# Optimization experiments

Hardware: AMD Instinct MI355X
Metric: run time of the kernel (lower is better)

The kernel has to match this reference:

```python
import jax, jax.numpy as jnp
import numpy as np

B, H, W = 128, 64, 64
MAP = 128          # gff mapping_dim
GFF_SCALE = 10.0   # common default scale for Gaussian Fourier features


def _ku(k, shape, fan_in):
    # torch kaiming_uniform_(a=sqrt(5)) -> bound = 1/sqrt(fan_in)
    b = 1.0 / np.sqrt(fan_in)
    return jax.random.uniform(k, shape, jnp.float32, -b, b)


def setup_inputs() -> dict:
    key = jax.random.key(0)
    ks = jax.random.split(key, 16)
    coords = jax.random.uniform(ks[0], (B, 2, H, W), jnp.float32)
    Bmat = GFF_SCALE * jax.random.normal(ks[1], (2, MAP), jnp.float32)
    # FMMLinear(256, 256_out? no) -- linear1: in=256, out=256, rank=70
    L1 = _ku(ks[2], (256, 70), 70)
    R1 = _ku(ks[3], (70, 256), 256)
    b1 = jax.random.uniform(ks[4], (256,), jnp.float32, -1/np.sqrt(256), 1/np.sqrt(256))
    # linear2: in=256, out=128, rank=10
    L2 = _ku(ks[5], (128, 10), 10)
    R2 = _ku(ks[6], (10, 256), 256)
    b2 = jax.random.uniform(ks[7], (128,), jnp.float32, -1/np.sqrt(256), 1/np.sqrt(256))
    # dense layers (torch nn.Linear default init)
    W3 = _ku(ks[8], (32, 128), 128)
    b3 = jax.random.uniform(ks[9], (32,), jnp.float32, -1/np.sqrt(128), 1/np.sqrt(128))
    W4 = _ku(ks[10], (16, 32), 32)
    b4 = jax.random.uniform(ks[11], (16,), jnp.float32, -1/np.sqrt(32), 1/np.sqrt(32))
    W5 = _ku(ks[12], (3, 16), 16)
    b5 = jax.random.uniform(ks[13], (3,), jnp.float32, -1/np.sqrt(16), 1/np.sqrt(16))
    return dict(coords=coords, Bmat=Bmat, L1=L1, R1=R1, b1=b1,
                L2=L2, R2=R2, b2=b2, W3=W3, b3=b3, W4=W4, b4=b4, W5=W5, b5=b5)


def reference(coords, Bmat, L1, R1, b1, L2, R2, b2, W3, b3, W4, b4, W5, b5):
    # Gaussian Fourier features: [B,2,H,W] -> [B,H,W,2*MAP]
    proj = (2.0 * jnp.pi) * jnp.einsum('bchw,cm->bhwm', coords, Bmat)
    x = jnp.concatenate([jnp.sin(proj), jnp.cos(proj)], axis=-1)
    x = x.reshape(-1, 2 * MAP)                       # (b h w) c
    x = jax.nn.relu(x @ (L1 @ R1).T + b1)            # FMM linear1
    x = jax.nn.relu(x @ (L2 @ R2).T + b2)            # FMM linear2
    x = jax.nn.relu(x @ W3.T + b3)
    x = jax.nn.relu(x @ W4.T + b4)
    out = (x @ W5.T + b5)[None]                      # [1, B*H*W, 3]
    return out
```

## Files before the change

kernel.cpp:

```cpp
#include <hip/hip_runtime.h>


typedef __attribute__((ext_vector_type(8))) short bf16x8;
typedef __attribute__((ext_vector_type(4))) float f32x4;
typedef __attribute__((ext_vector_type(4))) int i32x4;

__device__ inline unsigned short f2bf(float f) {
  unsigned u = __float_as_uint(f);
  return (unsigned short)((u + 0x7FFFu + ((u >> 16) & 1u)) >> 16);
}
__device__ inline unsigned short f2bf_fast(float f) {
  return (unsigned short)((__float_as_uint(f) + 0x8000u) >> 16);
}
__device__ inline unsigned packbf(float s, float c) {
  return (unsigned)((__float_as_uint(s) + 0x8000u) >> 16) |
         ((__float_as_uint(c) + 0x8000u) & 0xFFFF0000u);
}

__global__ __launch_bounds__(256) void prep_pack(
    const float* __restrict__ R1, const float* __restrict__ L1,
    const float* __restrict__ R2, const float* __restrict__ L2,
    const float* __restrict__ W3, const float* __restrict__ W4,
    void* __restrict__ ws) {
  unsigned short* w16 = (unsigned short*)ws;
  float* wf = (float*)ws;
  int e = blockIdx.x * 256 + threadIdx.x;
  if (e < 20480) {
    int kt = e / 2560, rem = e % 2560;
    int n = rem >> 5, oj = rem & 31;
    int k = kt * 32 + oj;
    int feat = (k & 1) ? 128 + (k >> 1) : (k >> 1);
    w16[e] = f2bf((n < 70) ? R1[n * 256 + feat] : 0.0f);
  } else if (e < 45056) {
    int f = e - 20480;
    int kt = f / 8192, rem = f % 8192;
    int n = rem >> 5, oj = rem & 31;
    int k = kt * 32 + oj;
    w16[e] = f2bf((k < 70) ? L1[n * 70 + k] : 0.0f);
  } else if (e < 49152) {
    int f = e - 45056;
    int kt = f / 512, rem = f % 512;
    int n = rem >> 5, k = kt * 32 + (rem & 31);
    w16[e] = f2bf((n < 10) ? R2[n * 256 + k] : 0.0f);
  } else if (e < 53248) {
    int f = e - 49152;
    int j = f & 7, h = (f >> 3) & 3, n = (f >> 5) & 15, nt = f >> 9;
    int k = h * 8 + j;
    w16[e] = f2bf((k < 10) ? L2[(nt * 16 + n) * 10 + k] : 0.0f);
  } else if (e < 57344) {
    int f = e - 53248;
    int j = f & 7, h = (f >> 3) & 3, n = (f >> 5) & 15;
    int nt2 = (f >> 9) & 1, rd = f >> 10;
    w16[e] = f2bf(W3[(nt2 * 16 + n) * 128 + rd * 32 + h * 8 + j]);
  } else if (e < 57856) {
    int h2 = e - 57344;
    int q = h2 >> 4, p = h2 & 15;
    wf[28672 + h2] = W4[p * 32 + q];
  }
}

__global__ __launch_bounds__(64, 2) void mlp_mfma(
    const float* __restrict__ coords, const float* __restrict__ Bm,
    const float* __restrict__ b1, const float* __restrict__ b2,
    const float* __restrict__ b3v, const float* __restrict__ b4v,
    const float* __restrict__ W5, const float* __restrict__ b5,
    const void* __restrict__ ws, float* __restrict__ out) {
  const int l = threadIdx.x;
  const int lo = l & 15, hi = l >> 4;
  const int pix0 = blockIdx.x * 64;

  __shared__ __align__(16) char smem[13312];
  unsigned short* Y16 = (unsigned short*)smem;
  unsigned short* X16 = (unsigned short*)smem;
  unsigned short* Z16 = (unsigned short*)(smem + 5632);
  float* O3f = (float*)smem;

  const unsigned short* R1p = (const unsigned short*)ws;
  const unsigned short* L1p = ((const unsigned short*)ws) + 20480;
  const unsigned short* R2p = ((const unsigned short*)ws) + 45056;
  const unsigned short* L2p = ((const unsigned short*)ws) + 49152;
  const unsigned short* W3p = ((const unsigned short*)ws) + 53248;
  const float* W4T = ((const float*)ws) + 28672;

  const f32x4 fz = {0.0f, 0.0f, 0.0f, 0.0f};

  float c0m[4], c1m[4];
#pragma unroll
  for (int mt = 0; mt < 4; ++mt) {
    int p = pix0 + mt * 16 + lo;
    int bb = p >> 12, hw = p & 4095;
    c0m[mt] = coords[bb * 8192 + hw];
    c1m[mt] = coords[bb * 8192 + 4096 + hw];
  }

  f32x4 y[4][5];
#pragma unroll
  for (int mt = 0; mt < 4; ++mt)
#pragma unroll
    for (int nt = 0; nt < 5; ++nt) y[mt][nt] = fz;

  float bm0[4], bm1[4];
#pragma unroll
  for (int p = 0; p < 4; ++p) {
    int m = hi * 4 + p;
    bm0[p] = Bm[m]; bm1[p] = Bm[128 + m];
  }
  for (int kt = 0; kt < 8; ++kt) {
    float nb0[4], nb1[4];
    if (kt < 7) {
#pragma unroll
      for (int p = 0; p < 4; ++p) {
        int m = (kt + 1) * 16 + hi * 4 + p;
        nb0[p] = Bm[m]; nb1[p] = Bm[128 + m];
      }
    }
    bf16x8 bfr[5];
#pragma unroll
    for (int nt = 0; nt < 5; ++nt)
      bfr[nt] = *(const bf16x8*)(R1p + ((kt * 80 + nt * 16 + lo) * 4 + hi) * 8);
    bf16x8 af[4];
#pragma unroll
    for (int mt = 0; mt < 4; ++mt) {
#pragma unroll
      for (int p = 0; p < 4; ++p) {
        float u = fmaf(c0m[mt], bm0[p], c1m[mt] * bm1[p]);
        float t = u - floorf(u);
        float s = __builtin_amdgcn_sinf(t);
        float c = __builtin_amdgcn_cosf(t);
        ((unsigned*)&af[mt])[p] = packbf(s, c);
      }
    }
#pragma unroll
    for (int mt = 0; mt < 4; ++mt)
#pragma unroll
      for (int nt = 0; nt < 5; ++nt)
        y[mt][nt] = __builtin_amdgcn_mfma_f32_16x16x32_bf16(af[mt], bfr[nt],
                                                            y[mt][nt], 0, 0, 0);
#pragma unroll
    for (int p = 0; p < 4; ++p) { bm0[p] = nb0[p]; bm1[p] = nb1[p]; }
  }

#pragma unroll
  for (int mt = 0; mt < 4; ++mt)
#pragma unroll
    for (int nt = 0; nt < 5; ++nt)
#pragma unroll
      for (int r = 0; r < 4; ++r)
        Y16[(mt * 16 + hi * 4 + r) * 104 + nt * 16 + lo] = f2bf_fast(y[mt][nt][r]);
  *(i32x4*)(Y16 + l * 104 + 80) = (i32x4){0, 0, 0, 0};
  *(i32x4*)(Y16 + l * 104 + 88) = (i32x4){0, 0, 0, 0};
  __syncthreads();

  bf16x8 ay[4][3];
#pragma unroll
  for (int mt = 0; mt < 4; ++mt)
#pragma unroll
    for (int kt = 0; kt < 3; ++kt)
      ay[mt][kt] = *(const bf16x8*)(Y16 + (mt * 16 + lo) * 104 + kt * 32 + hi * 8);
  __syncthreads();

  f32x4 zfr[4];
#pragma unroll
  for (int mt = 0; mt < 4; ++mt) zfr[mt] = fz;

  bf16x8 blc[3];
#pragma unroll
  for (int kt = 0; kt < 3; ++kt)
    blc[kt] = *(const bf16x8*)(L1p + ((kt * 256 + lo) * 4 + hi) * 8);

#pragma unroll 2
  for (int nt = 0; nt < 16; ++nt) {
    bf16x8 bln[3];
    if (nt < 15) {
#pragma unroll
      for (int kt = 0; kt < 3; ++kt)
        bln[kt] = *(const bf16x8*)(L1p + ((kt * 256 + (nt + 1) * 16 + lo) * 4 + hi) * 8);
    }
    float bias = b1[nt * 16 + lo];
    f32x4 cf[4];
#pragma unroll
    for (int mt = 0; mt < 4; ++mt) cf[mt] = fz;
#pragma unroll
    for (int kt = 0; kt < 3; ++kt)
#pragma unroll
      for (int mt = 0; mt < 4; ++mt)
        cf[mt] = __builtin_amdgcn_mfma_f32_16x16x32_bf16(ay[mt][kt], blc[kt],
                                                         cf[mt], 0, 0, 0);
#pragma unroll
    for (int mt = 0; mt < 4; ++mt)
#pragma unroll
      for (int r = 0; r < 4; ++r)
        X16[(mt * 16 + hi * 4 + r) * 40 + (nt & 1) * 16 + lo] =
            f2bf_fast(fmaxf(cf[mt][r] + bias, 0.0f));
    if (nt & 1) {
      __syncthreads();
      int rd = nt >> 1;
      bf16x8 br = *(const bf16x8*)(R2p + ((rd * 16 + lo) * 4 + hi) * 8);
#pragma unroll
      for (int mt = 0; mt < 4; ++mt) {
        bf16x8 aa = *(const bf16x8*)(X16 + (mt * 16 + lo) * 40 + hi * 8);
        zfr[mt] = __builtin_amdgcn_mfma_f32_16x16x32_bf16(aa, br, zfr[mt],
                                                          0, 0, 0);
      }
      __syncthreads();
    }
#pragma unroll
    for (int kt = 0; kt < 3; ++kt) blc[kt] = bln[kt];
  }

#pragma unroll
  for (int mt = 0; mt < 4; ++mt)
#pragma unroll
    for (int r = 0; r < 4; ++r)
      Z16[(mt * 16 + hi * 4 + r) * 32 + lo] = f2bf_fast(zfr[mt][r]);
  *(i32x4*)(Z16 + l * 32 + 16) = (i32x4){0, 0, 0, 0};
  *(i32x4*)(Z16 + l * 32 + 24) = (i32x4){0, 0, 0, 0};
  __syncthreads();
  bf16x8 az[4];
#pragma unroll
  for (int mt = 0; mt < 4; ++mt)
    az[mt] = *(const bf16x8*)(Z16 + (mt * 16 + lo) * 32 + hi * 8);
  __syncthreads();

  f32x4 o3fr[4][2];
#pragma unroll
  for (int mt = 0; mt < 4; ++mt) { o3fr[mt][0] = fz; o3fr[mt][1] = fz; }

  bf16x8 wlc = *(const bf16x8*)(L2p + (lo * 4 + hi) * 8);
#pragma unroll 2
  for (int nt = 0; nt < 8; ++nt) {
    bf16x8 wln;
    if (nt < 7)
      wln = *(const bf16x8*)(L2p + (((nt + 1) * 16 + lo) * 4 + hi) * 8);
    float bias = b2[nt * 16 + lo];
    f32x4 cf[4];
#pragma unroll
    for (int mt = 0; mt < 4; ++mt)
      cf[mt] = __builtin_amdgcn_mfma_f32_16x16x32_bf16(az[mt], wlc, fz, 0, 0, 0);
#pragma unroll
    for (int mt = 0; mt < 4; ++mt)
#pragma unroll
      for (int r = 0; r < 4; ++r)
        X16[(mt * 16 + hi * 4 + r) * 40 + (nt & 1) * 16 + lo] =
            f2bf_fast(fmaxf(cf[mt][r] + bias, 0.0f));
    if (nt & 1) {
      __syncthreads();
      int rd = nt >> 1;
      bf16x8 aa[4];
#pragma unroll
      for (int mt = 0; mt < 4; ++mt)
        aa[mt] = *(const bf16x8*)(X16 + (mt * 16 + lo) * 40 + hi * 8);
#pragma unroll
      for (int nt2 = 0; nt2 < 2; ++nt2) {
        bf16x8 bw = *(const bf16x8*)(W3p + (((rd * 2 + nt2) * 16 + lo) * 4 + hi) * 8);
#pragma unroll
        for (int mt = 0; mt < 4; ++mt)
          o3fr[mt][nt2] = __builtin_amdgcn_mfma_f32_16x16x32_bf16(
              aa[mt], bw, o3fr[mt][nt2], 0, 0, 0);
      }
      __syncthreads();
    }
    wlc = wln;
  }

#pragma unroll
  for (int mt = 0; mt < 4; ++mt)
#pragma unroll
    for (int nt2 = 0; nt2 < 2; ++nt2)
#pragma unroll
      for (int r = 0; r < 4; ++r)
        O3f[(mt * 16 + hi * 4 + r) * 33 + nt2 * 16 + lo] =
            fmaxf(o3fr[mt][nt2][r] + b3v[nt2 * 16 + lo], 0.0f);
  __syncthreads();

  float o3l[32];
#pragma unroll
  for (int q = 0; q < 32; ++q) o3l[q] = O3f[l * 33 + q];

  float o4[16];
#pragma unroll
  for (int p = 0; p < 16; ++p) o4[p] = b4v[p];
#pragma unroll
  for (int q = 0; q < 32; ++q) {
    float a = o3l[q];
    const float* __restrict__ w4 = W4T + q * 16;
#pragma unroll
    for (int p = 0; p < 16; ++p) o4[p] = fmaf(a, w4[p], o4[p]);
  }
#pragma unroll
  for (int p = 0; p < 16; ++p) o4[p] = fmaxf(o4[p], 0.0f);

#pragma unroll
  for (int e = 0; e < 3; ++e) {
    float acc = b5[e];
    const float* __restrict__ w5 = W5 + e * 16;
#pragma unroll
    for (int p = 0; p < 16; ++p) acc = fmaf(o4[p], w5[p], acc);
    out[(pix0 + l) * 3 + e] = acc;
  }
}

extern "C" void kernel_launch(void* const* d_in, const int* in_sizes, int n_in,
                              void* d_out, int out_size, void* d_ws, size_t ws_size,
                              hipStream_t stream) {
  const float* coords = (const float*)d_in[0];
  const float* Bmat   = (const float*)d_in[1];
  const float* L1     = (const float*)d_in[2];
  const float* R1     = (const float*)d_in[3];
  const float* b1     = (const float*)d_in[4];
  const float* L2     = (const float*)d_in[5];
  const float* R2     = (const float*)d_in[6];
  const float* b2     = (const float*)d_in[7];
  const float* W3     = (const float*)d_in[8];
  const float* b3     = (const float*)d_in[9];
  const float* W4     = (const float*)d_in[10];
  const float* b4     = (const float*)d_in[11];
  const float* W5     = (const float*)d_in[12];
  const float* b5     = (const float*)d_in[13];

  prep_pack<<<227, 256, 0, stream>>>(R1, L1, R2, L2, W3, W4, d_ws);
  mlp_mfma<<<8192, 64, 0, stream>>>(coords, Bmat, b1, b2, b3, b4, W5, b5,
                                    d_ws, (float*)d_out);
}
```

Before: 168.2 us.

## Replace block barriers with per-wave LDS fences and pack bf16 pairs with hardware cvt

Each block now holds two independent waves, and each wave gets its own LDS slice. Because the slices are private, __syncthreads is replaced by s_waitcnt lgkmcnt(0) fences. The weight packing is permuted so that adjacent column pairs interleave, which lets results be written as packed bf16 pairs using the hardware cvt_pk_bf16_f32 when it is available. The intermediate Y tile shrinks by being staged in two passes, and the layer-1 and layer-2 loops now process even and odd column tiles together, double-buffering the X tile. The goals are fewer barriers, fewer LDS stores and higher occupancy. The costs are reliance on wave-local fence semantics, more register pressure, and rounding that may differ slightly from the old software conversion.

Result: slower. 296.5 us (+76.3%).

```diff
diff --git a/kernel.cpp b/kernel.cpp
--- a/kernel.cpp
+++ b/kernel.cpp
@@ -5,17 +5,25 @@
 typedef __attribute__((ext_vector_type(4))) float f32x4;
 typedef __attribute__((ext_vector_type(4))) int i32x4;
 
+#define LFENCE() asm volatile("s_waitcnt lgkmcnt(0)" ::: "memory")
+
 __device__ inline unsigned short f2bf(float f) {
   unsigned u = __float_as_uint(f);
   return (unsigned short)((u + 0x7FFFu + ((u >> 16) & 1u)) >> 16);
 }
-__device__ inline unsigned short f2bf_fast(float f) {
-  return (unsigned short)((__float_as_uint(f) + 0x8000u) >> 16);
-}
-__device__ inline unsigned packbf(float s, float c) {
-  return (unsigned)((__float_as_uint(s) + 0x8000u) >> 16) |
-         ((__float_as_uint(c) + 0x8000u) & 0xFFFF0000u);
-}
+
+#if __has_builtin(__builtin_amdgcn_cvt_pk_bf16_f32)
+typedef __attribute__((ext_vector_type(2))) __bf16 bf16x2;
+__device__ inline unsigned pk2bf(float a, float b) {
+  bf16x2 v = __builtin_amdgcn_cvt_pk_bf16_f32(a, b);
+  return __builtin_bit_cast(unsigned, v);
+}
+#else
+__device__ inline unsigned pk2bf(float a, float b) {
+  return ((__float_as_uint(a) + 0x8000u) >> 16) |
+         ((__float_as_uint(b) + 0x8000u) & 0xFFFF0000u);
+}
+#endif
 
 __global__ __launch_bounds__(256) void prep_pack(
     const float* __restrict__ R1, const float* __restrict__ L1,
@@ -35,13 +43,14 @@
     int f = e - 20480;
     int kt = f / 8192, rem = f % 8192;
     int n = rem >> 5, oj = rem & 31;
-    int k = kt * 32 + oj;
-    w16[e] = f2bf((k < 70) ? L1[n * 70 + k] : 0.0f);
+    int r = kt * 32 + (oj & 1) * 16 + (oj >> 1);
+    w16[e] = f2bf((r < 70) ? L1[n * 70 + r] : 0.0f);
   } else if (e < 49152) {
-    int f = e - 45056;
-    int kt = f / 512, rem = f % 512;
-    int n = rem >> 5, k = kt * 32 + (rem & 31);
-    w16[e] = f2bf((n < 10) ? R2[n * 256 + k] : 0.0f);
+    int g = e - 45056;
+    int rd = g / 512, rem = g % 512;
+    int n = rem >> 5, oj = rem & 31;
+    int j = rd * 32 + (oj & 1) * 16 + (oj >> 1);
+    w16[e] = f2bf((n < 10) ? R2[n * 256 + j] : 0.0f);
   } else if (e < 53248) {
     int f = e - 49152;
     int j = f & 7, h = (f >> 3) & 3, n = (f >> 5) & 15, nt = f >> 9;
@@ -49,9 +58,9 @@
     w16[e] = f2bf((k < 10) ? L2[(nt * 16 + n) * 10 + k] : 0.0f);
   } else if (e < 57344) {
     int f = e - 53248;
-    int j = f & 7, h = (f >> 3) & 3, n = (f >> 5) & 15;
-    int nt2 = (f >> 9) & 1, rd = f >> 10;
-    w16[e] = f2bf(W3[(nt2 * 16 + n) * 128 + rd * 32 + h * 8 + j]);
+    int oj = f & 31, n = (f >> 5) & 15, nt2 = (f >> 9) & 1, rd = f >> 10;
+    int i = rd * 32 + (oj & 1) * 16 + (oj >> 1);
+    w16[e] = f2bf(W3[(nt2 * 16 + n) * 128 + i]);
   } else if (e < 57856) {
     int h2 = e - 57344;
     int q = h2 >> 4, p = h2 & 15;
@@ -59,21 +68,22 @@
   }
 }
 
-__global__ __launch_bounds__(64, 2) void mlp_mfma(
+__global__ __launch_bounds__(128, 4) void mlp_mfma(
     const float* __restrict__ coords, const float* __restrict__ Bm,
     const float* __restrict__ b1, const float* __restrict__ b2,
     const float* __restrict__ b3v, const float* __restrict__ b4v,
     const float* __restrict__ W5, const float* __restrict__ b5,
     const void* __restrict__ ws, float* __restrict__ out) {
-  const int l = threadIdx.x;
+  const int l = threadIdx.x & 63;
+  const int wv = threadIdx.x >> 6;
   const int lo = l & 15, hi = l >> 4;
-  const int pix0 = blockIdx.x * 64;
-
-  __shared__ __align__(16) char smem[13312];
-  unsigned short* Y16 = (unsigned short*)smem;
-  unsigned short* X16 = (unsigned short*)smem;
-  unsigned short* Z16 = (unsigned short*)(smem + 5632);
-  float* O3f = (float*)smem;
+  const int pix0 = blockIdx.x * 128 + wv * 64;
+
+  __shared__ __align__(16) char smem[20480];
+  char* slice = smem + wv * 10240;
+  unsigned short* Y16 = (unsigned short*)slice;
+  unsigned short* X16 = (unsigned short*)slice;
+  float* O3f = (float*)slice;
 
   const unsigned short* R1p = (const unsigned short*)ws;
   const unsigned short* L1p = ((const unsigned short*)ws) + 20480;
@@ -127,7 +137,7 @@
         float t = u - floorf(u);
         float s = __builtin_amdgcn_sinf(t);
         float c = __builtin_amdgcn_cosf(t);
-        ((unsigned*)&af[mt])[p] = packbf(s, c);
+        ((unsigned*)&af[mt])[p] = pk2bf(s, c);
       }
     }
 #pragma unroll
@@ -143,126 +153,131 @@
 #pragma unroll
   for (int mt = 0; mt < 4; ++mt)
 #pragma unroll
-    for (int nt = 0; nt < 5; ++nt)
-#pragma unroll
-      for (int r = 0; r < 4; ++r)
-        Y16[(mt * 16 + hi * 4 + r) * 104 + nt * 16 + lo] = f2bf_fast(y[mt][nt][r]);
-  *(i32x4*)(Y16 + l * 104 + 80) = (i32x4){0, 0, 0, 0};
-  *(i32x4*)(Y16 + l * 104 + 88) = (i32x4){0, 0, 0, 0};
-  __syncthreads();
-
+    for (int r = 0; r < 4; ++r) {
+      int row = mt * 16 + hi * 4 + r;
+      *(unsigned*)(Y16 + row * 72 + lo * 2)      = pk2bf(y[mt][0][r], y[mt][1][r]);
+      *(unsigned*)(Y16 + row * 72 + 32 + lo * 2) = pk2bf(y[mt][2][r], y[mt][3][r]);
+    }
+  LFENCE();
   bf16x8 ay[4][3];
 #pragma unroll
   for (int mt = 0; mt < 4; ++mt)
 #pragma unroll
+    for (int kt = 0; kt < 2; ++kt)
+      ay[mt][kt] = *(const bf16x8*)(Y16 + (mt * 16 + lo) * 72 + kt * 32 + hi * 8);
+  LFENCE();
+#pragma unroll
+  for (int mt = 0; mt < 4; ++mt)
+#pragma unroll
+    for (int r = 0; r < 4; ++r) {
+      int row = mt * 16 + hi * 4 + r;
+      *(unsigned*)(Y16 + row * 72 + lo * 2) = pk2bf(y[mt][4][r], 0.0f);
+    }
+  LFENCE();
+#pragma unroll
+  for (int mt = 0; mt < 4; ++mt)
+    ay[mt][2] = *(const bf16x8*)(Y16 + (mt * 16 + lo) * 72 + hi * 8);
+  LFENCE();
+
+  f32x4 zfr[4];
+#pragma unroll
+  for (int mt = 0; mt < 4; ++mt) zfr[mt] = fz;
+
+#pragma unroll
+  for (int rd = 0; rd < 8; ++rd) {
+    unsigned short* Xb = X16 + (rd & 1) * 2560;
+    bf16x8 blE[3], blO[3];
+#pragma unroll
+    for (int kt = 0; kt < 3; ++kt) {
+      blE[kt] = *(const bf16x8*)(L1p + ((kt * 256 + (2 * rd) * 16 + lo) * 4 + hi) * 8);
+      blO[kt] = *(const bf16x8*)(L1p + ((kt * 256 + (2 * rd + 1) * 16 + lo) * 4 + hi) * 8);
+    }
+    float biasE = b1[2 * rd * 16 + lo];
+    float biasO = b1[(2 * rd + 1) * 16 + lo];
+    f32x4 cfE[4], cfO[4];
+#pragma unroll
+    for (int mt = 0; mt < 4; ++mt) { cfE[mt] = fz; cfO[mt] = fz; }
+#pragma unroll
     for (int kt = 0; kt < 3; ++kt)
-      ay[mt][kt] = *(const bf16x8*)(Y16 + (mt * 16 + lo) * 104 + kt * 32 + hi * 8);
-  __syncthreads();
-
-  f32x4 zfr[4];
-#pragma unroll
-  for (int mt = 0; mt < 4; ++mt) zfr[mt] = fz;
-
-  bf16x8 blc[3];
-#pragma unroll
-  for (int kt = 0; kt < 3; ++kt)
-    blc[kt] = *(const bf16x8*)(L1p + ((kt * 256 + lo) * 4 + hi) * 8);
-
-#pragma unroll 2
-  for (int nt = 0; nt < 16; ++nt) {
-    bf16x8 bln[3];
-    if (nt < 15) {
-#pragma unroll
-      for (int kt = 0; kt < 3; ++kt)
-        bln[kt] = *(const bf16x8*)(L1p + ((kt * 256 + (nt + 1) * 16 + lo) * 4 + hi) * 8);
-    }
-    float bias = b1[nt * 16 + lo];
-    f32x4 cf[4];
-#pragma unroll
-    for (int mt = 0; mt < 4; ++mt) cf[mt] = fz;
-#pragma unroll
-    for (int kt = 0; kt < 3; ++kt)
-#pragma unroll
-      for (int mt = 0; mt < 4; ++mt)
-        cf[mt] = __builtin_amdgcn_mfma_f32_16x16x32_bf16(ay[mt][kt], blc[kt],
-                                                         cf[mt], 0, 0, 0);
+#pragma unroll
+      for (int mt = 0; mt < 4; ++mt) {
+        cfE[mt] = __builtin_amdgcn_mfma_f32_16x16x32_bf16(ay[mt][kt], blE[kt],
+                                                          cfE[mt], 0, 0, 0);
+        cfO[mt] = __builtin_amdgcn_mfma_f32_16x16x32_bf16(ay[mt][kt], blO[kt],
+                                                          cfO[mt], 0, 0, 0);
+      }
 #pragma unroll
     for (int mt = 0; mt < 4; ++mt)
 #pragma unroll
-      for (int r = 0; r < 4; ++r)
-        X16[(mt * 16 + hi * 4 + r) * 40 + (nt & 1) * 16 + lo] =
-            f2bf_fast(fmaxf(cf[mt][r] + bias, 0.0f));
-    if (nt & 1) {
-      __syncthreads();
-      int rd = nt >> 1;
-      bf16x8 br = *(const bf16x8*)(R2p + ((rd * 16 + lo) * 4 + hi) * 8);
-#pragma unroll
-      for (int mt = 0; mt < 4; ++mt) {
-        bf16x8 aa = *(const bf16x8*)(X16 + (mt * 16 + lo) * 40 + hi * 8);
-        zfr[mt] = __builtin_amdgcn_mfma_f32_16x16x32_bf16(aa, br, zfr[mt],
-                                                          0, 0, 0);
-      }
-      __syncthreads();
-    }
-#pragma unroll
-    for (int kt = 0; kt < 3; ++kt) blc[kt] = bln[kt];
-  }
-
+      for (int r = 0; r < 4; ++r) {
+        float v0 = fmaxf(cfE[mt][r] + biasE, 0.0f);
+        float v1 = fmaxf(cfO[mt][r] + biasO, 0.0f);
+        *(unsigned*)(Xb + (mt * 16 + hi * 4 + r) * 40 + lo * 2) = pk2bf(v0, v1);
+      }
+    LFENCE();
+    bf16x8 br = *(const bf16x8*)(R2p + (rd * 16 + lo) * 32 + hi * 8);
+#pragma unroll
+    for (int mt = 0; mt < 4; ++mt) {
+      bf16x8 aa = *(const bf16x8*)(Xb + (mt * 16 + lo) * 40 + hi * 8);
+      zfr[mt] = __builtin_amdgcn_mfma_f32_16x16x32_bf16(aa, br, zfr[mt], 0, 0, 0);
+    }
+  }
+
+  unsigned short* Z16 = X16;
 #pragma unroll
   for (int mt = 0; mt < 4; ++mt)
 #pragma unroll
     for (int r = 0; r < 4; ++r)
-      Z16[(mt * 16 + hi * 4 + r) * 32 + lo] = f2bf_fast(zfr[mt][r]);
-  *(i32x4*)(Z16 + l * 32 + 16) = (i32x4){0, 0, 0, 0};
-  *(i32x4*)(Z16 + l * 32 + 24) = (i32x4){0, 0, 0, 0};
-  __syncthreads();
+      Z16[(mt * 16 + hi * 4 + r) * 40 + lo] =
+          (unsigned short)(pk2bf(zfr[mt][r], 0.0f) & 0xFFFFu);
+  *(i32x4*)(Z16 + l * 40 + 16) = (i32x4){0, 0, 0, 0};
+  *(i32x4*)(Z16 + l * 40 + 24) = (i32x4){0, 0, 0, 0};
+  LFENCE();
   bf16x8 az[4];
 #pragma unroll
   for (int mt = 0; mt < 4; ++mt)
-    az[mt] = *(const bf16x8*)(Z16 + (mt * 16 + lo) * 32 + hi * 8);
-  __syncthreads();
+    az[mt] = *(const bf16x8*)(Z16 + (mt * 16 + lo) * 40 + hi * 8);
+  LFENCE();
 
   f32x4 o3fr[4][2];
 #pragma unroll
   for (int mt = 0; mt < 4; ++mt) { o3fr[mt][0] = fz; o3fr[mt][1] = fz; }
 
-  bf16x8 wlc = *(const bf16x8*)(L2p + (lo * 4 + hi) * 8);
-#pragma unroll 2
-  for (int nt = 0; nt < 8; ++nt) {
-    bf16x8 wln;
-    if (nt < 7)
-      wln = *(const bf16x8*)(L2p + (((nt + 1) * 16 + lo) * 4 + hi) * 8);
-    float bias = b2[nt * 16 + lo];
-    f32x4 cf[4];
+#pragma unroll
+  for (int rd = 0; rd < 4; ++rd) {
+    unsigned short* Xb = X16 + (rd & 1) * 2560;
+    bf16x8 wlE = *(const bf16x8*)(L2p + ((2 * rd) * 16 + lo) * 32 + hi * 8);
+    bf16x8 wlO = *(const bf16x8*)(L2p + ((2 * rd + 1) * 16 + lo) * 32 + hi * 8);
+    float biasE = b2[2 * rd * 16 + lo];
+    float biasO = b2[(2 * rd + 1) * 16 + lo];
+    f32x4 cfE[4], cfO[4];
+#pragma unroll
+    for (int mt = 0; mt < 4; ++mt) {
+      cfE[mt] = __builtin_amdgcn_mfma_f32_16x16x32_bf16(az[mt], wlE, fz, 0, 0, 0);
+      cfO[mt] = __builtin_amdgcn_mfma_f32_16x16x32_bf16(az[mt], wlO, fz, 0, 0, 0);
+    }
 #pragma unroll
     for (int mt = 0; mt < 4; ++mt)
-      cf[mt] = __builtin_amdgcn_mfma_f32_16x16x32_bf16(az[mt], wlc, fz, 0, 0, 0);
-#pragma unroll
-    for (int mt = 0; mt < 4; ++mt)
-#pragma unroll
-      for (int r = 0; r < 4; ++r)
-        X16[(mt * 16 + hi * 4 + r) * 40 + (nt & 1) * 16 + lo] =
-            f2bf_fast(fmaxf(cf[mt][r] + bias, 0.0f));
-    if (nt & 1) {
-      __syncthreads();
-      int rd = nt >> 1;
-      bf16x8 aa[4];
-#pragma unroll
-      for (int mt = 0; mt < 4; ++mt)
-        aa[mt] = *(const bf16x8*)(X16 + (mt * 16 + lo) * 40 + hi * 8);
-#pragma unroll
-      for (int nt2 = 0; nt2 < 2; ++nt2) {
-        bf16x8 bw = *(const bf16x8*)(W3p + (((rd * 2 + nt2) * 16 + lo) * 4 + hi) * 8);
-#pragma unroll
-        for (int mt = 0; mt < 4; ++mt)
-          o3fr[mt][nt2] = __builtin_amdgcn_mfma_f32_16x16x32_bf16(
-              aa[mt], bw, o3fr[mt][nt2], 0, 0, 0);
-      }
-      __syncthreads();
-    }
-    wlc = wln;
-  }
-
+#pragma unroll
+      for (int r = 0; r < 4; ++r) {
+        float v0 = fmaxf(cfE[mt][r] + biasE, 0.0f);
+        float v1 = fmaxf(cfO[mt][r] + biasO, 0.0f);
+        *(unsigned*)(Xb + (mt * 16 + hi * 4 + r) * 40 + lo * 2) = pk2bf(v0, v1);
+      }
+    LFENCE();
+    bf16x8 bw0 = *(const bf16x8*)(W3p + ((rd * 2 + 0) * 16 + lo) * 32 + hi * 8);
+    bf16x8 bw1 = *(const bf16x8*)(W3p + ((rd * 2 + 1) * 16 + lo) * 32 + hi * 8);
+#pragma unroll
+    for (int mt = 0; mt < 4; ++mt) {
+      bf16x8 aa = *(const bf16x8*)(Xb + (mt * 16 + lo) * 40 + hi * 8);
+      o3fr[mt][0] = __builtin_amdgcn_mfma_f32_16x16x32_bf16(aa, bw0, o3fr[mt][0],
+                                                            0, 0, 0);
+      o3fr[mt][1] = __builtin_amdgcn_mfma_f32_16x16x32_bf16(aa, bw1, o3fr[mt][1],
+                                                            0, 0, 0);
+    }
+  }
+
+  LFENCE();
 #pragma unroll
   for (int mt = 0; mt < 4; ++mt)
 #pragma unroll
@@ -271,7 +286,7 @@
       for (int r = 0; r < 4; ++r)
         O3f[(mt * 16 + hi * 4 + r) * 33 + nt2 * 16 + lo] =
             fmaxf(o3fr[mt][nt2][r] + b3v[nt2 * 16 + lo], 0.0f);
-  __syncthreads();
+  LFENCE();
 
   float o3l[32];
 #pragma unroll
@@ -319,6 +334,6 @@
   const float* b5     = (const float*)d_in[13];
 
   prep_pack<<<227, 256, 0, stream>>>(R1, L1, R2, L2, W3, W4, d_ws);
-  mlp_mfma<<<8192, 64, 0, stream>>>(coords, Bmat, b1, b2, b3, b4, W5, b5,
-                                    d_ws, (float*)d_out);
-}
+  mlp_mfma<<<4096, 128, 0, stream>>>(coords, Bmat, b1, b2, b3, b4, W5, b5,
+                                     d_ws, (float*)d_out);
+}
```
